# Optimization experiments

Hardware: AMD Instinct MI355X
Metric: run time of the kernel (lower is better)

The kernel has to match this reference:

```python
import jax, jax.numpy as jnp
import numpy as np

MUL = 32            # multiplicity of each irrep (0e and 1o)
N_NODES = 50000
N_EDGES = 800000
NUM_NEIGHBORS = 16.0
SQRT3 = 3.0 ** 0.5
SILU_NORM = 1.6790  # e3nn normalize2mom constant for silu: 1/sqrt(E[silu(z)^2]), z~N(0,1)


def split_irreps(x):
    # x: [..., 128] laid out as 32x0e (32) ++ 32x1o (32*3)
    x0 = x[..., :MUL]
    x1 = x[..., MUL:].reshape(x.shape[:-1] + (MUL, 3))
    return x0, x1


def merge_irreps(x0, x1):
    return jnp.concatenate([x0, x1.reshape(x1.shape[:-2] + (MUL * 3,))], axis=-1)


def fctp_scalar(x0, x1, a, W0, W1, fan_in):
    # FullyConnectedTensorProduct(in_irreps, '1x0e', out_irreps): per-irrep linear
    # mixing scaled by scalar attr; e3nn path weight sqrt(dim_out/fan_in) times the
    # orthonormal CG (1/sqrt(dim)) folds to 1/sqrt(fan_in) for every irrep.
    s = a / jnp.sqrt(jnp.asarray(fan_in, x0.dtype))
    o0 = (x0 @ W0) * s
    o1 = jnp.einsum('nud,uw->nwd', x1, W1) * s[..., None]
    return o0, o1


def setup_inputs() -> dict:
    key = jax.random.key(0)
    ks = jax.random.split(key, 17)
    inp = dict(
        node_input=jax.random.normal(ks[0], (N_NODES, 4 * MUL), jnp.float32),
        node_attr=jnp.ones((N_NODES, 1), jnp.float32),
        edge_src=jax.random.randint(ks[1], (N_EDGES,), 0, N_NODES),
        edge_dst=jax.random.randint(ks[2], (N_EDGES,), 0, N_NODES),
        edge_attr=jax.random.normal(ks[3], (N_EDGES, 4), jnp.float32),
        edge_scalars=jax.random.normal(ks[4], (N_EDGES, 64), jnp.float32),
    )
    p = lambda k, sh: jax.random.normal(k, sh, jnp.float32)  # e3nn init: N(0,1)
    inp.update(
        W_sc0=p(ks[5], (MUL, MUL)), W_sc1=p(ks[6], (MUL, MUL)),
        W_l1_0=p(ks[7], (MUL, MUL)), W_l1_1=p(ks[8], (MUL, MUL)),
        W_fc1=p(ks[9], (64, 64)), W_fc2=p(ks[10], (64, 4 * MUL)),
        W_l2_A0=p(ks[11], (MUL, MUL)), W_l2_B0=p(ks[12], (MUL, MUL)),
        W_l2_C1=p(ks[13], (MUL, MUL)), W_l2_D1=p(ks[14], (MUL, MUL)),
        W_l3_A=p(ks[15], (MUL, 1)), W_l3_B=p(ks[16], (MUL, 1)),
    )
    return inp


def reference(node_input, node_attr, edge_src, edge_dst, edge_attr, edge_scalars,
              W_sc0, W_sc1, W_l1_0, W_l1_1, W_fc1, W_fc2,
              W_l2_A0, W_l2_B0, W_l2_C1, W_l2_D1, W_l3_A, W_l3_B):
    n = node_input.shape[0]
    x0, x1 = split_irreps(node_input)

    # per-edge TP weights from MLP on edge scalars (e3nn FullyConnectedNet)
    h = SILU_NORM * jax.nn.silu(edge_scalars @ (W_fc1 / 8.0))  # /sqrt(64)
    weight = h @ (W_fc2 / 8.0)                                  # [E, 128]

    # self connection (sc) and lin1 (FCTP with scalar node attr, fan_in = 32)
    sc0, sc1 = fctp_scalar(x0, x1, node_attr, W_sc0, W_sc1, MUL)
    f0, f1 = fctp_scalar(x0, x1, node_attr, W_l1_0, W_l1_1, MUL)

    # gather source-node features per edge
    g0 = f0[edge_src]          # [E, 32]
    g1 = f1[edge_src]          # [E, 32, 3]
    e0 = edge_attr[:, :1]      # [E, 1]  0e
    e1 = edge_attr[:, 1:]      # [E, 3]  1o

    # weight layout follows instruction order: (0e*0e->0e), (0e*1o->1o), (1o*0e->1o), (1o*1o->0e)
    wA, wC, wD, wB = (weight[:, :MUL], weight[:, MUL:2 * MUL],
                      weight[:, 2 * MUL:3 * MUL], weight[:, 3 * MUL:])
    # weighted CG tensor product ('uvu'); e3nn path weights sqrt(dim_out) folded with
    # orthonormal wigner-3j entries (1/sqrt(3) for l=1 couplings)
    outA = wA * g0 * e0                                    # [E,32]   0e x 0e -> 0e
    outB = wB * jnp.einsum('euk,ek->eu', g1, e1) / SQRT3   # [E,32]   1o x 1o -> 0e
    outC = (wC * g0)[..., None] * e1[:, None, :]           # [E,32,3] 0e x 1o -> 1o
    outD = wD[..., None] * g1 * e0[..., None]              # [E,32,3] 1o x 0e -> 1o

    # scatter-add aggregation to destination nodes
    seg = lambda v: jax.ops.segment_sum(v, edge_dst, num_segments=n)
    inv = 1.0 / jnp.sqrt(jnp.asarray(NUM_NEIGHBORS, node_input.dtype))
    mA, mB, mC, mD = seg(outA) * inv, seg(outB) * inv, seg(outC) * inv, seg(outD) * inv

    # lin2: irreps_mid (32x0e+32x0e+32x1o+32x1o) -> output, fan_in = 64 per output irrep
    s = node_attr / 8.0  # attr / sqrt(64)
    c0 = (mA @ W_l2_A0 + mB @ W_l2_B0) * s
    c1 = (jnp.einsum('nud,uw->nwd', mC, W_l2_C1)
          + jnp.einsum('nud,uw->nwd', mD, W_l2_D1)) * s[..., None]

    # lin3: irreps_mid -> 0e gate angle (only 0e chunks contribute)
    angle = 0.1 * (mA @ W_l3_A + mB @ W_l3_B) * s          # [N, 1]
    cos, sin = jnp.cos(angle), jnp.sin(angle)              # sc.output_mask is all ones

    return cos * merge_irreps(sc0, sc1) + sin * merge_irreps(c0, c1)
```

## Files before the change

### kernel.cpp

```cpp
#include <hip/hip_runtime.h>
#include <stdint.h>

#define N_NODES 50000
#define N_EDGES 800000
#define CAP 64
#define NTILES 50000
#define NSB 49

typedef _Float16 f16x8 __attribute__((ext_vector_type(8)));
typedef _Float16 f16x2 __attribute__((ext_vector_type(2)));
typedef float    f32x4 __attribute__((ext_vector_type(4)));

struct F3 { float x, y, z; };

static __device__ __forceinline__ uint32_t pk16(float a, float b) {
    return __builtin_bit_cast(uint32_t, __builtin_amdgcn_cvt_pkrtz(a, b));
}
static __device__ __forceinline__ float lo16(uint32_t v) {
    f16x2 h = __builtin_bit_cast(f16x2, v); return (float)h[0];
}
static __device__ __forceinline__ float hi16(uint32_t v) {
    f16x2 h = __builtin_bit_cast(f16x2, v); return (float)h[1];
}

__global__ __launch_bounds__(256) void k_node_f(
        const float* __restrict__ x, const float* __restrict__ attr,
        const float* __restrict__ W0, const float* __restrict__ W1,
        const float* __restrict__ Wsc0, const float* __restrict__ Wsc1,
        uint32_t* __restrict__ fh, uint32_t* __restrict__ sch)
{
    const int wv = threadIdx.x >> 6;
    const int t  = threadIdx.x & 63;
    const int node = blockIdx.x*4 + wv;
    if (node >= N_NODES) return;
    __shared__ float xs[4][128];
    xs[wv][t]      = x[(size_t)node*128 + t];
    xs[wv][64 + t] = x[(size_t)node*128 + 64 + t];
    float a = attr[node] * 0.17677669529663689f;

    float s0 = 0.f, s1 = 0.f;
    if (t < 32) {
        #pragma unroll
        for (int v = 0; v < 32; ++v) {
            s0 += xs[wv][v] * W0[v*32 + t];
            s1 += xs[wv][32 + v*3 + 0] * W1[v*32 + t];
        }
    } else {
        int u = t - 32;
        #pragma unroll
        for (int v = 0; v < 32; ++v) {
            s0 += xs[wv][32 + v*3 + 1] * W1[v*32 + u];
            s1 += xs[wv][32 + v*3 + 2] * W1[v*32 + u];
        }
    }
    fh[(size_t)node*64 + t] = pk16(s0*a, s1*a);

    float c0 = 0.f, c1 = 0.f;
    if (t < 32) {
        #pragma unroll
        for (int v = 0; v < 32; ++v) c0 += xs[wv][v] * Wsc0[v*32 + t];
    } else {
        int cc = t - 32, w = cc / 3, d = cc - 3*w;
        #pragma unroll
        for (int v = 0; v < 32; ++v) c0 += xs[wv][32 + v*3 + d] * Wsc1[v*32 + w];
    }
    {
        int cc = t + 32;
        int w = cc / 3, d = cc - 3*w;
        #pragma unroll
        for (int v = 0; v < 32; ++v) c1 += xs[wv][32 + v*3 + d] * Wsc1[v*32 + w];
    }
    sch[(size_t)node*64 + t] = pk16(c0*a, c1*a);
}

__global__ void k_ticket(const int* __restrict__ dst, int* __restrict__ cnt,
                         uint8_t* __restrict__ slot8) {
    int e = blockIdx.x*256 + threadIdx.x;
    if (e >= N_EDGES) return;
    int d = dst[e];
    int slot = atomicAdd(&cnt[d], 1);
    slot8[e] = (uint8_t)min(slot, 255);
}

__global__ __launch_bounds__(1024) void k_scan1(const int* __restrict__ cnt,
                                                int* __restrict__ offs,
                                                int* __restrict__ bsum) {
    __shared__ int sh[1024];
    int t = threadIdx.x, i = blockIdx.x*1024 + t;
    int v = (i < N_NODES) ? min(cnt[i], CAP) : 0;
    sh[t] = v; __syncthreads();
    #pragma unroll
    for (int off = 1; off < 1024; off <<= 1) {
        int u = (t >= off) ? sh[t - off] : 0;
        __syncthreads();
        sh[t] += u;
        __syncthreads();
    }
    if (i < N_NODES) offs[i] = sh[t] - v;
    if (t == 1023) bsum[blockIdx.x] = sh[t];
}

__global__ void k_scan2(const int* __restrict__ bsum, int* __restrict__ bbase,
                        int* __restrict__ offs) {
    int t = threadIdx.x;
    int v = (t < NSB) ? bsum[t] : 0;
    int inc = v;
    #pragma unroll
    for (int off = 1; off < 64; off <<= 1) {
        int u = __shfl_up(inc, off);
        if (t >= off) inc += u;
    }
    if (t < NSB) bbase[t] = inc - v;
    if (t == NSB - 1) offs[N_NODES] = inc;
}

__global__ __launch_bounds__(1024) void k_scan3(int* __restrict__ offs,
                                                const int* __restrict__ bbase) {
    int i = blockIdx.x*1024 + threadIdx.x;
    if (i < N_NODES) offs[i] += bbase[blockIdx.x];
}

__global__ void k_scatter(const int* __restrict__ dst, const int* __restrict__ esrc,
                          const float* __restrict__ eattr,
                          const uint8_t* __restrict__ slot8,
                          const int* __restrict__ offs,
                          int2* __restrict__ csr_se, F3* __restrict__ csr_e1) {
    int e = blockIdx.x*256 + threadIdx.x;
    if (e >= N_EDGES) return;
    int slot = slot8[e];
    if (slot >= CAP) return;
    int pos = offs[dst[e]] + slot;
    csr_se[pos] = make_int2(e, esrc[e]);
    float4 ea = *(const float4*)(eattr + (size_t)e*4);
    csr_e1[pos] = {ea.y, ea.z, ea.w};
}

__global__ __launch_bounds__(256) void k_edge_w(
    const float* __restrict__ escal, const float* __restrict__ eattr,
    const float* __restrict__ Wfc1, const float* __restrict__ Wfc2,
    uint32_t* __restrict__ weight)
{
    __shared__ __align__(16) _Float16 lds_h[4][16][72];
    __shared__ __align__(16) uint32_t lds_o[4][16][68];

    const int wv   = threadIdx.x >> 6;
    const int lane = threadIdx.x & 63;
    const int rl   = lane & 15;
    const int g4   = lane >> 4;

    f16x8 w1f[2][4];
    #pragma unroll
    for (int ks = 0; ks < 2; ++ks)
      #pragma unroll
      for (int jt = 0; jt < 4; ++jt)
        #pragma unroll
        for (int i = 0; i < 8; ++i)
          w1f[ks][jt][i] = (_Float16)(Wfc1[(ks*32 + g4*8 + i)*64 + jt*16 + rl] * 0.125f);
    f16x8 w2f[2][8];
    #pragma unroll
    for (int ks = 0; ks < 2; ++ks)
      #pragma unroll
      for (int jt = 0; jt < 8; ++jt)
        #pragma unroll
        for (int i = 0; i < 8; ++i)
          w2f[ks][jt][i] = (_Float16)(Wfc2[(ks*32 + g4*8 + i)*128 + jt*16 + rl] * 0.125f);

    const int w  = blockIdx.x*4 + wv;
    const int t0 = w*8;
    const int t1 = (t0 + 8 < NTILES) ? t0 + 8 : NTILES;

    for (int tt = t0; tt < t1; ++tt) {
        const int eb = tt*16;
        f16x8 af[2];
        #pragma unroll
        for (int ks = 0; ks < 2; ++ks) {
            const float* p = escal + (size_t)(eb + rl)*64 + ks*32 + g4*8;
            float4 lo = *(const float4*)(p);
            float4 hi = *(const float4*)(p + 4);
            uint32_t pk[4] = { pk16(lo.x, lo.y), pk16(lo.z, lo.w),
                               pk16(hi.x, hi.y), pk16(hi.z, hi.w) };
            af[ks] = __builtin_bit_cast(f16x8, *(uint4*)pk);
        }
        float e0L = eattr[(size_t)(eb + rl)*4];

        f32x4 hacc[4];
        #pragma unroll
        for (int jt = 0; jt < 4; ++jt) {
            f32x4 z = {0.f,0.f,0.f,0.f};
            z = __builtin_amdgcn_mfma_f32_16x16x32_f16(af[0], w1f[0][jt], z, 0,0,0);
            z = __builtin_amdgcn_mfma_f32_16x16x32_f16(af[1], w1f[1][jt], z, 0,0,0);
            hacc[jt] = z;
        }
        #pragma unroll
        for (int jt = 0; jt < 4; ++jt)
          #pragma unroll
          for (int r = 0; r < 4; ++r) {
            float v = hacc[jt][r];
            float s = 1.679f * v / (1.f + __expf(-v));
            lds_h[wv][g4*4 + r][jt*16 + rl] = (_Float16)s;
          }
        f16x8 a2[2];
        #pragma unroll
        for (int ks = 0; ks < 2; ++ks)
            a2[ks] = *reinterpret_cast<const f16x8*>(&lds_h[wv][rl][ks*32 + g4*8]);

        f32x4 z[8];
        #pragma unroll
        for (int jt = 0; jt < 8; ++jt) {
            f32x4 zz = {0.f,0.f,0.f,0.f};
            zz = __builtin_amdgcn_mfma_f32_16x16x32_f16(a2[0], w2f[0][jt], zz, 0,0,0);
            zz = __builtin_amdgcn_mfma_f32_16x16x32_f16(a2[1], w2f[1][jt], zz, 0,0,0);
            z[jt] = zz;
        }

        #pragma unroll
        for (int pg = 0; pg < 2; ++pg)
          #pragma unroll
          for (int r = 0; r < 4; ++r) {
            float e0r = __shfl(e0L, g4*4 + r);
            float loA = z[pg][r]     * (0.25f * e0r);
            float hiC = z[2 + pg][r] * 0.25f;
            float loD = z[4 + pg][r] * (0.25f * e0r);
            float hiB = z[6 + pg][r] * 0.14433756729740643f;
            lds_o[wv][g4*4 + r][pg*16 + rl]      = pk16(loA, hiC);
            lds_o[wv][g4*4 + r][32 + pg*16 + rl] = pk16(loD, hiB);
          }

        const int qr = lane >> 4;
        const int ql = lane & 15;
        #pragma unroll
        for (int it = 0; it < 4; ++it) {
            int r = it*4 + qr;
            *(uint4*)(weight + (size_t)(eb + r)*64 + ql*4) =
                *(const uint4*)(&lds_o[wv][r][ql*4]);
        }
    }
}

__global__ __launch_bounds__(256, 6) void k_main(
    const float* __restrict__ attr,
    const uint32_t* __restrict__ weight, const int2* __restrict__ csr_se,
    const F3* __restrict__ csr_e1,
    const float* __restrict__ WA0,  const float* __restrict__ WB0,
    const float* __restrict__ WC1,  const float* __restrict__ WD1,
    const float* __restrict__ W3A,  const float* __restrict__ W3B,
    const uint32_t* __restrict__ fh, const uint32_t* __restrict__ sch,
    const int* __restrict__ offs,   float* __restrict__ out)
{
    __shared__ float lds_m[4][256];
    __shared__ float2 lds_p[4];

    const int wv   = threadIdx.x >> 6;
    const int lane = threadIdx.x & 63;
    const int u    = lane & 31;
    const int half = lane >> 5;
    const int node = blockIdx.x*4 + wv;

    const int o0  = __builtin_amdgcn_readfirstlane(offs[node]);
    const int deg = __builtin_amdgcn_readfirstlane(offs[node + 1]) - o0;

    float mAB = 0.f, mCD0 = 0.f, mCD1 = 0.f, mCD2 = 0.f;

    for (int b = 0; b < deg; b += 16) {
        int nb = min(16, deg - b);
        uint32_t wp[16], ga[16], gbv[16];
        #pragma unroll
        for (int j = 0; j < 16; ++j) if (j < nb) {
            int pos = o0 + b + j;
            int2 se = csr_se[pos];
            wp[j] = weight[(size_t)se.x*64 + lane];
            const uint32_t* fr = fh + (size_t)se.y*64;
            ga[j] = fr[u];
            if (half) gbv[j] = fr[32 + u];
        }
        #pragma unroll
        for (int j = 0; j < 16; ++j) if (j < nb) {
            int pos = o0 + b + j;
            F3 v = csr_e1[pos];
            float e1x = v.x, e1y = v.y, e1z = v.z;
            float lo = lo16(wp[j]), hi = hi16(wp[j]);
            if (half == 0) {
                float g0 = lo16(ga[j]);
                mAB += lo * g0;
                float tc = hi * g0;
                mCD0 += tc*e1x; mCD1 += tc*e1y; mCD2 += tc*e1z;
            } else {
                float gx = hi16(ga[j]);
                float gy = lo16(gbv[j]), gz = hi16(gbv[j]);
                mAB += hi * (gx*e1x + gy*e1y + gz*e1z);
                mCD0 += lo*gx; mCD1 += lo*gy; mCD2 += lo*gz;
            }
        }
    }

    float* M = lds_m[wv];
    if (half == 0) {
        M[u] = mAB;
        M[64  + u*3 + 0] = mCD0; M[64  + u*3 + 1] = mCD1; M[64  + u*3 + 2] = mCD2;
    } else {
        M[32 + u] = mAB;
        M[160 + u*3 + 0] = mCD0; M[160 + u*3 + 1] = mCD1; M[160 + u*3 + 2] = mCD2;
    }

    float a  = attr[node];
    float a8 = a * 0.125f;
    const float w3 = (half == 0) ? W3A[u] : W3B[u];
    float tpart = (half == 0) ? M[u] * w3 : M[32 + u] * w3;
    #pragma unroll
    for (int off = 32; off > 0; off >>= 1) tpart += __shfl_xor(tpart, off);
    float angle = 0.1f * tpart * a8;
    float sn, cs; __sincosf(angle, &sn, &cs);
    if (lane == 0) lds_p[wv] = make_float2(cs, sn * a8);
    __syncthreads();

    const int t   = threadIdx.x;
    const int c   = t & 127;
    const int grp = t >> 7;
    const float* M0 = lds_m[grp*2 + 0];
    const float* M1 = lds_m[grp*2 + 1];
    bool A = (c < 32);
    int cc = c - 32;
    int wq = cc / 3, d = cc - 3*wq;
    int b1 = A ? 0  : 64 + d;
    int b2 = A ? 32 : 160 + d;
    int sT = A ? 1 : 3;
    const float* pWa = (A ? WA0 : WC1) + (A ? c : wq);
    const float* pWb = (A ? WB0 : WD1) + (A ? c : wq);
    float sa = 0.f, sb = 0.f;
    #pragma unroll
    for (int uu = 0; uu < 32; ++uu) {
        float wa = pWa[uu*32], wb = pWb[uu*32];
        sa += M0[b1 + uu*sT] * wa + M0[b2 + uu*sT] * wb;
        sb += M1[b1 + uu*sT] * wa + M1[b2 + uu*sT] * wb;
    }
    int n0 = blockIdx.x*4 + grp*2;
    float2 p0 = lds_p[grp*2 + 0], p1 = lds_p[grp*2 + 1];
    uint32_t sp0 = sch[(size_t)n0*64 + (c & 63)];
    uint32_t sp1 = sch[(size_t)(n0 + 1)*64 + (c & 63)];
    float sc0 = (c < 64) ? lo16(sp0) : hi16(sp0);
    float sc1 = (c < 64) ? lo16(sp1) : hi16(sp1);
    out[(size_t)n0*128 + c]       = p0.x*sc0 + p0.y*sa;
    out[(size_t)(n0 + 1)*128 + c] = p1.x*sc1 + p1.y*sb;
}

extern "C" void kernel_launch(void* const* d_in, const int* in_sizes, int n_in,
                              void* d_out, int out_size, void* d_ws, size_t ws_size,
                              hipStream_t stream) {
    const float* node_input = (const float*)d_in[0];
    const float* node_attr  = (const float*)d_in[1];
    const int*   edge_src   = (const int*)  d_in[2];
    const int*   edge_dst   = (const int*)  d_in[3];
    const float* edge_attr  = (const float*)d_in[4];
    const float* edge_scal  = (const float*)d_in[5];
    const float* W_sc0 = (const float*)d_in[6];
    const float* W_sc1 = (const float*)d_in[7];
    const float* W_l10 = (const float*)d_in[8];
    const float* W_l11 = (const float*)d_in[9];
    const float* W_fc1 = (const float*)d_in[10];
    const float* W_fc2 = (const float*)d_in[11];
    const float* W_A0  = (const float*)d_in[12];
    const float* W_B0  = (const float*)d_in[13];
    const float* W_C1  = (const float*)d_in[14];
    const float* W_D1  = (const float*)d_in[15];
    const float* W_3A  = (const float*)d_in[16];
    const float* W_3B  = (const float*)d_in[17];
    float* out = (float*)d_out;

    char* p = (char*)d_ws;
    auto alloc = [&](size_t bytes) { char* r = p; p += (bytes + 15) & ~(size_t)15; return r; };
    uint32_t* fh      = (uint32_t*)alloc((size_t)N_NODES*64*4);
    int*      cnt     = (int*)     alloc((size_t)N_NODES*4);
    int*      offs    = (int*)     alloc((size_t)(N_NODES+1)*4);
    uint8_t*  slot8   = (uint8_t*) alloc((size_t)N_EDGES);
    int*      bsum    = (int*)     alloc((size_t)NSB*4);
    int*      bbase   = (int*)     alloc((size_t)NSB*4);
    int2*     csr_se  = (int2*)    alloc((size_t)N_EDGES*8);
    F3*       csr_e1  = (F3*)      alloc((size_t)N_EDGES*12);
    uint32_t* weight  = (uint32_t*)alloc((size_t)N_EDGES*64*4);
    uint32_t* sch     = (uint32_t*)alloc((size_t)N_NODES*64*4);

    hipMemsetAsync(cnt, 0, (size_t)N_NODES*4, stream);
    k_node_f <<<(N_NODES+3)/4, 256, 0, stream>>>(node_input, node_attr, W_l10, W_l11,
               W_sc0, W_sc1, fh, sch);
    k_ticket <<<(N_EDGES+255)/256, 256, 0, stream>>>(edge_dst, cnt, slot8);
    k_scan1  <<<NSB, 1024, 0, stream>>>(cnt, offs, bsum);
    k_scan2  <<<1, 64, 0, stream>>>(bsum, bbase, offs);
    k_scan3  <<<NSB, 1024, 0, stream>>>(offs, bbase);
    k_scatter<<<(N_EDGES+255)/256, 256, 0, stream>>>(edge_dst, edge_src, edge_attr,
               slot8, offs, csr_se, csr_e1);
    k_edge_w <<<1563, 256, 0, stream>>>(edge_scal, edge_attr, W_fc1, W_fc2, weight);
    k_main   <<<(N_NODES+3)/4, 256, 0, stream>>>(node_attr, weight, csr_se, csr_e1,
               W_A0, W_B0, W_C1, W_D1, W_3A, W_3B, fh, sch, offs, out);
}
```

Before: 387.5 us.

## Fuse edge-weight MLP, CSR scatter and node transform into one block-partitioned kernel

Combines three independent kernels (edge MLP weight generation, CSR scatter, node linear/self-connection) into one launch whose blocks branch on block index into the three roles. This removes two kernel launches and lets the independent work overlap on the GPU instead of serialising. In exchange, every block reserves the union of shared memory, and register pressure follows the heaviest branch (the MFMA edge path), which can lower occupancy for the light scatter and node blocks.

```diff
diff --git a/kernel.cpp b/kernel.cpp
--- a/kernel.cpp
+++ b/kernel.cpp
@@ -7,6 +7,10 @@
 #define NTILES 50000
 #define NSB 49
 
+#define NB_EW 1563
+#define NB_SC 3125
+#define NB_NF 12500
+
 typedef _Float16 f16x8 __attribute__((ext_vector_type(8)));
 typedef _Float16 f16x2 __attribute__((ext_vector_type(2)));
 typedef float    f32x4 __attribute__((ext_vector_type(4)));
@@ -21,56 +25,6 @@
 }
 static __device__ __forceinline__ float hi16(uint32_t v) {
     f16x2 h = __builtin_bit_cast(f16x2, v); return (float)h[1];
-}
-
-__global__ __launch_bounds__(256) void k_node_f(
-        const float* __restrict__ x, const float* __restrict__ attr,
-        const float* __restrict__ W0, const float* __restrict__ W1,
-        const float* __restrict__ Wsc0, const float* __restrict__ Wsc1,
-        uint32_t* __restrict__ fh, uint32_t* __restrict__ sch)
-{
-    const int wv = threadIdx.x >> 6;
-    const int t  = threadIdx.x & 63;
-    const int node = blockIdx.x*4 + wv;
-    if (node >= N_NODES) return;
-    __shared__ float xs[4][128];
-    xs[wv][t]      = x[(size_t)node*128 + t];
-    xs[wv][64 + t] = x[(size_t)node*128 + 64 + t];
-    float a = attr[node] * 0.17677669529663689f;
-
-    float s0 = 0.f, s1 = 0.f;
-    if (t < 32) {
-        #pragma unroll
-        for (int v = 0; v < 32; ++v) {
-            s0 += xs[wv][v] * W0[v*32 + t];
-            s1 += xs[wv][32 + v*3 + 0] * W1[v*32 + t];
-        }
-    } else {
-        int u = t - 32;
-        #pragma unroll
-        for (int v = 0; v < 32; ++v) {
-            s0 += xs[wv][32 + v*3 + 1] * W1[v*32 + u];
-            s1 += xs[wv][32 + v*3 + 2] * W1[v*32 + u];
-        }
-    }
-    fh[(size_t)node*64 + t] = pk16(s0*a, s1*a);
-
-    float c0 = 0.f, c1 = 0.f;
-    if (t < 32) {
-        #pragma unroll
-        for (int v = 0; v < 32; ++v) c0 += xs[wv][v] * Wsc0[v*32 + t];
-    } else {
-        int cc = t - 32, w = cc / 3, d = cc - 3*w;
-        #pragma unroll
-        for (int v = 0; v < 32; ++v) c0 += xs[wv][32 + v*3 + d] * Wsc1[v*32 + w];
-    }
-    {
-        int cc = t + 32;
-        int w = cc / 3, d = cc - 3*w;
-        #pragma unroll
-        for (int v = 0; v < 32; ++v) c1 += xs[wv][32 + v*3 + d] * Wsc1[v*32 + w];
-    }
-    sch[(size_t)node*64 + t] = pk16(c0*a, c1*a);
 }
 
 __global__ void k_ticket(const int* __restrict__ dst, int* __restrict__ cnt,
@@ -120,119 +74,174 @@
     if (i < N_NODES) offs[i] += bbase[blockIdx.x];
 }
 
-__global__ void k_scatter(const int* __restrict__ dst, const int* __restrict__ esrc,
-                          const float* __restrict__ eattr,
-                          const uint8_t* __restrict__ slot8,
-                          const int* __restrict__ offs,
-                          int2* __restrict__ csr_se, F3* __restrict__ csr_e1) {
-    int e = blockIdx.x*256 + threadIdx.x;
-    if (e >= N_EDGES) return;
-    int slot = slot8[e];
-    if (slot >= CAP) return;
-    int pos = offs[dst[e]] + slot;
-    csr_se[pos] = make_int2(e, esrc[e]);
-    float4 ea = *(const float4*)(eattr + (size_t)e*4);
-    csr_e1[pos] = {ea.y, ea.z, ea.w};
-}
-
-__global__ __launch_bounds__(256) void k_edge_w(
+__global__ __launch_bounds__(256) void k_fusedB(
     const float* __restrict__ escal, const float* __restrict__ eattr,
     const float* __restrict__ Wfc1, const float* __restrict__ Wfc2,
-    uint32_t* __restrict__ weight)
+    uint32_t* __restrict__ weight,
+    const int* __restrict__ edst, const int* __restrict__ esrc,
+    const uint8_t* __restrict__ slot8, const int* __restrict__ offs,
+    int2* __restrict__ csr_se, F3* __restrict__ csr_e1,
+    const float* __restrict__ x, const float* __restrict__ attr,
+    const float* __restrict__ W0, const float* __restrict__ W1,
+    const float* __restrict__ Wsc0, const float* __restrict__ Wsc1,
+    uint32_t* __restrict__ fh, uint32_t* __restrict__ sch)
 {
-    __shared__ __align__(16) _Float16 lds_h[4][16][72];
-    __shared__ __align__(16) uint32_t lds_o[4][16][68];
-
+    __shared__ __align__(16) uint8_t smem[26624];
+
+    const int bid  = blockIdx.x;
     const int wv   = threadIdx.x >> 6;
     const int lane = threadIdx.x & 63;
-    const int rl   = lane & 15;
-    const int g4   = lane >> 4;
-
-    f16x8 w1f[2][4];
-    #pragma unroll
-    for (int ks = 0; ks < 2; ++ks)
-      #pragma unroll
-      for (int jt = 0; jt < 4; ++jt)
-        #pragma unroll
-        for (int i = 0; i < 8; ++i)
-          w1f[ks][jt][i] = (_Float16)(Wfc1[(ks*32 + g4*8 + i)*64 + jt*16 + rl] * 0.125f);
-    f16x8 w2f[2][8];
-    #pragma unroll
-    for (int ks = 0; ks < 2; ++ks)
-      #pragma unroll
-      for (int jt = 0; jt < 8; ++jt)
-        #pragma unroll
-        for (int i = 0; i < 8; ++i)
-          w2f[ks][jt][i] = (_Float16)(Wfc2[(ks*32 + g4*8 + i)*128 + jt*16 + rl] * 0.125f);
-
-    const int w  = blockIdx.x*4 + wv;
-    const int t0 = w*8;
-    const int t1 = (t0 + 8 < NTILES) ? t0 + 8 : NTILES;
-
-    for (int tt = t0; tt < t1; ++tt) {
-        const int eb = tt*16;
-        f16x8 af[2];
-        #pragma unroll
-        for (int ks = 0; ks < 2; ++ks) {
-            const float* p = escal + (size_t)(eb + rl)*64 + ks*32 + g4*8;
-            float4 lo = *(const float4*)(p);
-            float4 hi = *(const float4*)(p + 4);
-            uint32_t pk[4] = { pk16(lo.x, lo.y), pk16(lo.z, lo.w),
-                               pk16(hi.x, hi.y), pk16(hi.z, hi.w) };
-            af[ks] = __builtin_bit_cast(f16x8, *(uint4*)pk);
-        }
-        float e0L = eattr[(size_t)(eb + rl)*4];
-
-        f32x4 hacc[4];
-        #pragma unroll
-        for (int jt = 0; jt < 4; ++jt) {
-            f32x4 z = {0.f,0.f,0.f,0.f};
-            z = __builtin_amdgcn_mfma_f32_16x16x32_f16(af[0], w1f[0][jt], z, 0,0,0);
-            z = __builtin_amdgcn_mfma_f32_16x16x32_f16(af[1], w1f[1][jt], z, 0,0,0);
-            hacc[jt] = z;
-        }
-        #pragma unroll
-        for (int jt = 0; jt < 4; ++jt)
-          #pragma unroll
-          for (int r = 0; r < 4; ++r) {
-            float v = hacc[jt][r];
-            float s = 1.679f * v / (1.f + __expf(-v));
-            lds_h[wv][g4*4 + r][jt*16 + rl] = (_Float16)s;
-          }
-        f16x8 a2[2];
+
+    if (bid < NB_EW) {
+        _Float16* H = (_Float16*)smem;
+        uint32_t* O = (uint32_t*)(smem + 9216);
+        const int rl = lane & 15;
+        const int g4 = lane >> 4;
+
+        f16x8 w1f[2][4];
         #pragma unroll
         for (int ks = 0; ks < 2; ++ks)
-            a2[ks] = *reinterpret_cast<const f16x8*>(&lds_h[wv][rl][ks*32 + g4*8]);
-
-        f32x4 z[8];
+          #pragma unroll
+          for (int jt = 0; jt < 4; ++jt)
+            #pragma unroll
+            for (int i = 0; i < 8; ++i)
+              w1f[ks][jt][i] = (_Float16)(Wfc1[(ks*32 + g4*8 + i)*64 + jt*16 + rl] * 0.125f);
+        f16x8 w2f[2][8];
         #pragma unroll
-        for (int jt = 0; jt < 8; ++jt) {
-            f32x4 zz = {0.f,0.f,0.f,0.f};
-            zz = __builtin_amdgcn_mfma_f32_16x16x32_f16(a2[0], w2f[0][jt], zz, 0,0,0);
-            zz = __builtin_amdgcn_mfma_f32_16x16x32_f16(a2[1], w2f[1][jt], zz, 0,0,0);
-            z[jt] = zz;
+        for (int ks = 0; ks < 2; ++ks)
+          #pragma unroll
+          for (int jt = 0; jt < 8; ++jt)
+            #pragma unroll
+            for (int i = 0; i < 8; ++i)
+              w2f[ks][jt][i] = (_Float16)(Wfc2[(ks*32 + g4*8 + i)*128 + jt*16 + rl] * 0.125f);
+
+        _Float16* Hw = H + wv*(16*72);
+        uint32_t* Ow = O + wv*(16*68);
+
+        const int w  = bid*4 + wv;
+        const int t0 = w*8;
+        const int t1 = (t0 + 8 < NTILES) ? t0 + 8 : NTILES;
+
+        for (int tt = t0; tt < t1; ++tt) {
+            const int eb = tt*16;
+            f16x8 af[2];
+            #pragma unroll
+            for (int ks = 0; ks < 2; ++ks) {
+                const float* p = escal + (size_t)(eb + rl)*64 + ks*32 + g4*8;
+                float4 lo = *(const float4*)(p);
+                float4 hi = *(const float4*)(p + 4);
+                uint32_t pk[4] = { pk16(lo.x, lo.y), pk16(lo.z, lo.w),
+                                   pk16(hi.x, hi.y), pk16(hi.z, hi.w) };
+                af[ks] = __builtin_bit_cast(f16x8, *(uint4*)pk);
+            }
+            float e0L = eattr[(size_t)(eb + rl)*4];
+
+            f32x4 hacc[4];
+            #pragma unroll
+            for (int jt = 0; jt < 4; ++jt) {
+                f32x4 z = {0.f,0.f,0.f,0.f};
+                z = __builtin_amdgcn_mfma_f32_16x16x32_f16(af[0], w1f[0][jt], z, 0,0,0);
+                z = __builtin_amdgcn_mfma_f32_16x16x32_f16(af[1], w1f[1][jt], z, 0,0,0);
+                hacc[jt] = z;
+            }
+            #pragma unroll
+            for (int jt = 0; jt < 4; ++jt)
+              #pragma unroll
+              for (int r = 0; r < 4; ++r) {
+                float v = hacc[jt][r];
+                float s = 1.679f * v / (1.f + __expf(-v));
+                Hw[(g4*4 + r)*72 + jt*16 + rl] = (_Float16)s;
+              }
+            f16x8 a2[2];
+            #pragma unroll
+            for (int ks = 0; ks < 2; ++ks)
+                a2[ks] = *reinterpret_cast<const f16x8*>(&Hw[rl*72 + ks*32 + g4*8]);
+
+            f32x4 z[8];
+            #pragma unroll
+            for (int jt = 0; jt < 8; ++jt) {
+                f32x4 zz = {0.f,0.f,0.f,0.f};
+                zz = __builtin_amdgcn_mfma_f32_16x16x32_f16(a2[0], w2f[0][jt], zz, 0,0,0);
+                zz = __builtin_amdgcn_mfma_f32_16x16x32_f16(a2[1], w2f[1][jt], zz, 0,0,0);
+                z[jt] = zz;
+            }
+
+            #pragma unroll
+            for (int pg = 0; pg < 2; ++pg)
+              #pragma unroll
+              for (int r = 0; r < 4; ++r) {
+                float e0r = __shfl(e0L, g4*4 + r);
+                float loA = z[pg][r]     * (0.25f * e0r);
+                float hiC = z[2 + pg][r] * 0.25f;
+                float loD = z[4 + pg][r] * (0.25f * e0r);
+                float hiB = z[6 + pg][r] * 0.14433756729740643f;
+                Ow[(g4*4 + r)*68 + pg*16 + rl]      = pk16(loA, hiC);
+                Ow[(g4*4 + r)*68 + 32 + pg*16 + rl] = pk16(loD, hiB);
+              }
+
+            const int qr = lane >> 4;
+            const int ql = lane & 15;
+            #pragma unroll
+            for (int it = 0; it < 4; ++it) {
+                int r = it*4 + qr;
+                *(uint4*)(weight + (size_t)(eb + r)*64 + ql*4) =
+                    *(const uint4*)(&Ow[r*68 + ql*4]);
+            }
         }
-
-        #pragma unroll
-        for (int pg = 0; pg < 2; ++pg)
-          #pragma unroll
-          for (int r = 0; r < 4; ++r) {
-            float e0r = __shfl(e0L, g4*4 + r);
-            float loA = z[pg][r]     * (0.25f * e0r);
-            float hiC = z[2 + pg][r] * 0.25f;
-            float loD = z[4 + pg][r] * (0.25f * e0r);
-            float hiB = z[6 + pg][r] * 0.14433756729740643f;
-            lds_o[wv][g4*4 + r][pg*16 + rl]      = pk16(loA, hiC);
-            lds_o[wv][g4*4 + r][32 + pg*16 + rl] = pk16(loD, hiB);
-          }
-
-        const int qr = lane >> 4;
-        const int ql = lane & 15;
-        #pragma unroll
-        for (int it = 0; it < 4; ++it) {
-            int r = it*4 + qr;
-            *(uint4*)(weight + (size_t)(eb + r)*64 + ql*4) =
-                *(const uint4*)(&lds_o[wv][r][ql*4]);
+    } else if (bid < NB_EW + NB_SC) {
+        int e = (bid - NB_EW)*256 + threadIdx.x;
+        if (e < N_EDGES) {
+            int slot = slot8[e];
+            if (slot < CAP) {
+                int pos = offs[edst[e]] + slot;
+                csr_se[pos] = make_int2(e, esrc[e]);
+                float4 ea = *(const float4*)(eattr + (size_t)e*4);
+                csr_e1[pos] = {ea.y, ea.z, ea.w};
+            }
+        }
+    } else {
+        float* XS = (float*)smem;
+        const int t = lane;
+        const int node = (bid - NB_EW - NB_SC)*4 + wv;
+        if (node < N_NODES) {
+            float* xsw = XS + wv*128;
+            xsw[t]      = x[(size_t)node*128 + t];
+            xsw[64 + t] = x[(size_t)node*128 + 64 + t];
+            float a = attr[node] * 0.17677669529663689f;
+
+            float s0 = 0.f, s1 = 0.f;
+            if (t < 32) {
+                #pragma unroll
+                for (int v = 0; v < 32; ++v) {
+                    s0 += xsw[v] * W0[v*32 + t];
+                    s1 += xsw[32 + v*3 + 0] * W1[v*32 + t];
+                }
+            } else {
+                int u = t - 32;
+                #pragma unroll
+                for (int v = 0; v < 32; ++v) {
+                    s0 += xsw[32 + v*3 + 1] * W1[v*32 + u];
+                    s1 += xsw[32 + v*3 + 2] * W1[v*32 + u];
+                }
+            }
+            fh[(size_t)node*64 + t] = pk16(s0*a, s1*a);
+
+            float c0 = 0.f, c1 = 0.f;
+            if (t < 32) {
+                #pragma unroll
+                for (int v = 0; v < 32; ++v) c0 += xsw[v] * Wsc0[v*32 + t];
+            } else {
+                int cc = t - 32, w = cc / 3, d = cc - 3*w;
+                #pragma unroll
+                for (int v = 0; v < 32; ++v) c0 += xsw[32 + v*3 + d] * Wsc1[v*32 + w];
+            }
+            {
+                int cc = t + 32;
+                int w = cc / 3, d = cc - 3*w;
+                #pragma unroll
+                for (int v = 0; v < 32; ++v) c1 += xsw[32 + v*3 + d] * Wsc1[v*32 + w];
+            }
+            sch[(size_t)node*64 + t] = pk16(c0*a, c1*a);
         }
     }
 }
@@ -380,15 +389,14 @@
     uint32_t* sch     = (uint32_t*)alloc((size_t)N_NODES*64*4);
 
     hipMemsetAsync(cnt, 0, (size_t)N_NODES*4, stream);
-    k_node_f <<<(N_NODES+3)/4, 256, 0, stream>>>(node_input, node_attr, W_l10, W_l11,
-               W_sc0, W_sc1, fh, sch);
     k_ticket <<<(N_EDGES+255)/256, 256, 0, stream>>>(edge_dst, cnt, slot8);
     k_scan1  <<<NSB, 1024, 0, stream>>>(cnt, offs, bsum);
     k_scan2  <<<1, 64, 0, stream>>>(bsum, bbase, offs);
     k_scan3  <<<NSB, 1024, 0, stream>>>(offs, bbase);
-    k_scatter<<<(N_EDGES+255)/256, 256, 0, stream>>>(edge_dst, edge_src, edge_attr,
-               slot8, offs, csr_se, csr_e1);
-    k_edge_w <<<1563, 256, 0, stream>>>(edge_scal, edge_attr, W_fc1, W_fc2, weight);
+    k_fusedB <<<NB_EW + NB_SC + NB_NF, 256, 0, stream>>>(
+               edge_scal, edge_attr, W_fc1, W_fc2, weight,
+               edge_dst, edge_src, slot8, offs, csr_se, csr_e1,
+               node_input, node_attr, W_l10, W_l11, W_sc0, W_sc1, fh, sch);
     k_main   <<<(N_NODES+3)/4, 256, 0, stream>>>(node_attr, weight, csr_se, csr_e1,
                W_A0, W_B0, W_C1, W_D1, W_3A, W_3B, fh, sch, offs, out);
 }
```

Result: no change. 395.2 us (+2.0%).

## Merge ticket and node-feature kernels, fold scan3 into consumers, raise k_main occupancy

Applied to the files above, without the earlier changes.

Merges the edge ticketing (atomic slot assignment) and the node feature projection into one launch, using block-index ranges to pick the role. It also drops the k_scan3 pass that added block bases to offsets. Instead, k_scatter and k_main each add bbase[idx>>10] when they read offsets. The aim is fewer kernel launches and less serialization. k_main's launch bounds move from 6 to 7 waves to raise occupancy, which adds register pressure and an extra small gather per read.

```diff
diff --git a/kernel.cpp b/kernel.cpp
--- a/kernel.cpp
+++ b/kernel.cpp
@@ -6,6 +6,8 @@
 #define CAP 64
 #define NTILES 50000
 #define NSB 49
+#define NB_TK 3125
+#define NB_NF 12500
 
 typedef _Float16 f16x8 __attribute__((ext_vector_type(8)));
 typedef _Float16 f16x2 __attribute__((ext_vector_type(2)));
@@ -23,17 +25,28 @@
     f16x2 h = __builtin_bit_cast(f16x2, v); return (float)h[1];
 }
 
-__global__ __launch_bounds__(256) void k_node_f(
-        const float* __restrict__ x, const float* __restrict__ attr,
-        const float* __restrict__ W0, const float* __restrict__ W1,
-        const float* __restrict__ Wsc0, const float* __restrict__ Wsc1,
-        uint32_t* __restrict__ fh, uint32_t* __restrict__ sch)
+__global__ __launch_bounds__(256) void k_fusedA(
+    const int* __restrict__ dst, int* __restrict__ cnt, uint8_t* __restrict__ slot8,
+    const float* __restrict__ x, const float* __restrict__ attr,
+    const float* __restrict__ W0, const float* __restrict__ W1,
+    const float* __restrict__ Wsc0, const float* __restrict__ Wsc1,
+    uint32_t* __restrict__ fh, uint32_t* __restrict__ sch)
 {
+    const int bid = blockIdx.x;
+    if (bid < NB_TK) {
+        int e = bid*256 + threadIdx.x;
+        if (e < N_EDGES) {
+            int d = dst[e];
+            int slot = atomicAdd(&cnt[d], 1);
+            slot8[e] = (uint8_t)min(slot, 255);
+        }
+        return;
+    }
+    __shared__ float xs[4][128];
     const int wv = threadIdx.x >> 6;
     const int t  = threadIdx.x & 63;
-    const int node = blockIdx.x*4 + wv;
+    const int node = (bid - NB_TK)*4 + wv;
     if (node >= N_NODES) return;
-    __shared__ float xs[4][128];
     xs[wv][t]      = x[(size_t)node*128 + t];
     xs[wv][64 + t] = x[(size_t)node*128 + 64 + t];
     float a = attr[node] * 0.17677669529663689f;
@@ -71,15 +84,6 @@
         for (int v = 0; v < 32; ++v) c1 += xs[wv][32 + v*3 + d] * Wsc1[v*32 + w];
     }
     sch[(size_t)node*64 + t] = pk16(c0*a, c1*a);
-}
-
-__global__ void k_ticket(const int* __restrict__ dst, int* __restrict__ cnt,
-                         uint8_t* __restrict__ slot8) {
-    int e = blockIdx.x*256 + threadIdx.x;
-    if (e >= N_EDGES) return;
-    int d = dst[e];
-    int slot = atomicAdd(&cnt[d], 1);
-    slot8[e] = (uint8_t)min(slot, 255);
 }
 
 __global__ __launch_bounds__(1024) void k_scan1(const int* __restrict__ cnt,
@@ -114,22 +118,17 @@
     if (t == NSB - 1) offs[N_NODES] = inc;
 }
 
-__global__ __launch_bounds__(1024) void k_scan3(int* __restrict__ offs,
-                                                const int* __restrict__ bbase) {
-    int i = blockIdx.x*1024 + threadIdx.x;
-    if (i < N_NODES) offs[i] += bbase[blockIdx.x];
-}
-
 __global__ void k_scatter(const int* __restrict__ dst, const int* __restrict__ esrc,
                           const float* __restrict__ eattr,
                           const uint8_t* __restrict__ slot8,
-                          const int* __restrict__ offs,
+                          const int* __restrict__ offs, const int* __restrict__ bbase,
                           int2* __restrict__ csr_se, F3* __restrict__ csr_e1) {
     int e = blockIdx.x*256 + threadIdx.x;
     if (e >= N_EDGES) return;
     int slot = slot8[e];
     if (slot >= CAP) return;
-    int pos = offs[dst[e]] + slot;
+    int d = dst[e];
+    int pos = offs[d] + bbase[d >> 10] + slot;
     csr_se[pos] = make_int2(e, esrc[e]);
     float4 ea = *(const float4*)(eattr + (size_t)e*4);
     csr_e1[pos] = {ea.y, ea.z, ea.w};
@@ -237,7 +236,7 @@
     }
 }
 
-__global__ __launch_bounds__(256, 6) void k_main(
+__global__ __launch_bounds__(256, 7) void k_main(
     const float* __restrict__ attr,
     const uint32_t* __restrict__ weight, const int2* __restrict__ csr_se,
     const F3* __restrict__ csr_e1,
@@ -245,7 +244,8 @@
     const float* __restrict__ WC1,  const float* __restrict__ WD1,
     const float* __restrict__ W3A,  const float* __restrict__ W3B,
     const uint32_t* __restrict__ fh, const uint32_t* __restrict__ sch,
-    const int* __restrict__ offs,   float* __restrict__ out)
+    const int* __restrict__ offs,   const int* __restrict__ bbase,
+    float* __restrict__ out)
 {
     __shared__ float lds_m[4][256];
     __shared__ float2 lds_p[4];
@@ -256,8 +256,10 @@
     const int half = lane >> 5;
     const int node = blockIdx.x*4 + wv;
 
-    const int o0  = __builtin_amdgcn_readfirstlane(offs[node]);
-    const int deg = __builtin_amdgcn_readfirstlane(offs[node + 1]) - o0;
+    const int o0 = __builtin_amdgcn_readfirstlane(offs[node] + bbase[node >> 10]);
+    const int i1 = node + 1;
+    int o1raw = (i1 == N_NODES) ? offs[N_NODES] : offs[i1] + bbase[i1 >> 10];
+    const int deg = __builtin_amdgcn_readfirstlane(o1raw) - o0;
 
     float mAB = 0.f, mCD0 = 0.f, mCD1 = 0.f, mCD2 = 0.f;
 
@@ -380,15 +382,13 @@
     uint32_t* sch     = (uint32_t*)alloc((size_t)N_NODES*64*4);
 
     hipMemsetAsync(cnt, 0, (size_t)N_NODES*4, stream);
-    k_node_f <<<(N_NODES+3)/4, 256, 0, stream>>>(node_input, node_attr, W_l10, W_l11,
-               W_sc0, W_sc1, fh, sch);
-    k_ticket <<<(N_EDGES+255)/256, 256, 0, stream>>>(edge_dst, cnt, slot8);
+    k_fusedA <<<NB_TK + NB_NF, 256, 0, stream>>>(edge_dst, cnt, slot8,
+               node_input, node_attr, W_l10, W_l11, W_sc0, W_sc1, fh, sch);
     k_scan1  <<<NSB, 1024, 0, stream>>>(cnt, offs, bsum);
     k_scan2  <<<1, 64, 0, stream>>>(bsum, bbase, offs);
-    k_scan3  <<<NSB, 1024, 0, stream>>>(offs, bbase);
     k_scatter<<<(N_EDGES+255)/256, 256, 0, stream>>>(edge_dst, edge_src, edge_attr,
-               slot8, offs, csr_se, csr_e1);
+               slot8, offs, bbase, csr_se, csr_e1);
     k_edge_w <<<1563, 256, 0, stream>>>(edge_scal, edge_attr, W_fc1, W_fc2, weight);
     k_main   <<<(N_NODES+3)/4, 256, 0, stream>>>(node_attr, weight, csr_se, csr_e1,
-               W_A0, W_B0, W_C1, W_D1, W_3A, W_3B, fh, sch, offs, out);
-}
+               W_A0, W_B0, W_C1, W_D1, W_3A, W_3B, fh, sch, offs, bbase, out);
+}
```

Result: faster. 374.9 us (-3.3%).
